# Performance work log

Hardware: AMD Instinct MI355X
Metric: run time of the kernel (lower is better)

## Reference

```python
import jax, jax.numpy as jnp
import numpy as np

B, N, D = 4, 2048, 1024

def setup_inputs() -> dict:
    key = jax.random.key(0)
    ks = jax.random.split(key, 8)
    s = 1.0 / np.sqrt(D)
    return {
        "x": jax.random.normal(ks[0], (B, N, D), dtype=jnp.float32),
        "Wq": jax.random.normal(ks[1], (D, D), dtype=jnp.float32) * s,
        "bq": jnp.zeros((D,), dtype=jnp.float32),
        "Wk": jax.random.normal(ks[2], (D, D), dtype=jnp.float32) * s,
        "bk": jnp.zeros((D,), dtype=jnp.float32),
        "Wv": jax.random.normal(ks[3], (D, D), dtype=jnp.float32) * s,
        "bv": jnp.zeros((D,), dtype=jnp.float32),
        "gamma": jnp.ones((1,), dtype=jnp.float32),
    }

def reference(x, Wq, bq, Wk, bk, Wv, bv, gamma):
    d = x.shape[-1]
    delta = 1.0 / jnp.sqrt(jnp.asarray(d, dtype=x.dtype))
    # torch Linear: y = x @ W.T + b, W is [out, in]
    Q = jnp.einsum('bnd,ed->bne', x, Wq) + bq
    K = jnp.einsum('bnd,ed->bne', x, Wk) + bk
    V = jnp.einsum('bnd,ed->bne', x, Wv) + bv
    scores = jnp.einsum('bne,bme->bnm', Q, K) * delta  # [B, N, N]
    attn = jax.nn.softmax(scores, axis=-1)
    out = jnp.einsum('bnm,bme->bne', attn, V)
    return out * gamma + x
```

## Files before the change

kernel.cpp:

```cpp
#include <hip/hip_runtime.h>

typedef _Float16 f16;
typedef __attribute__((ext_vector_type(4))) _Float16 f16x4;
typedef __attribute__((ext_vector_type(8))) _Float16 f16x8;
typedef __attribute__((ext_vector_type(4))) float f32x4;

#define B_ 4
#define N_ 2048
#define D_ 1024

__global__ __launch_bounds__(256) void k_cast_all(const float4* __restrict__ x,
                                                  const float4* __restrict__ wq,
                                                  const float4* __restrict__ wk,
                                                  const float4* __restrict__ wv,
                                                  f16x4* __restrict__ xo,
                                                  f16x4* __restrict__ wqo,
                                                  f16x4* __restrict__ wko,
                                                  f16x4* __restrict__ wvo,
                                                  float* __restrict__ rowsum) {
  int b = blockIdx.x;
  if (b >= 11264) {
    rowsum[(b - 11264) * 256 + threadIdx.x] = 0.f;
    return;
  }
  const float4* in;
  f16x4* out;
  int idx;
  if (b < 8192)       { in = x;  out = xo;  idx = b * 256 + threadIdx.x; }
  else if (b < 9216)  { in = wq; out = wqo; idx = (b - 8192) * 256 + threadIdx.x; }
  else if (b < 10240) { in = wk; out = wko; idx = (b - 9216) * 256 + threadIdx.x; }
  else                { in = wv; out = wvo; idx = (b - 10240) * 256 + threadIdx.x; }
  float4 v = in[idx];
  f16x4 o = { (_Float16)v.x, (_Float16)v.y, (_Float16)v.z, (_Float16)v.w };
  out[idx] = o;
}

__device__ __forceinline__ void stage_tile(const char* gRowBase, int rowStrideBytes,
                                           int kByte, char* lds, int tid) {
#pragma unroll
  for (int it = 0; it < 4; ++it) {
    int lin = it * 4096 + tid * 16;
    int row = lin >> 7;
    int pchunk = (lin >> 4) & 7;
    int lchunk = pchunk ^ (row & 7);
    const char* g = gRowBase + (long)row * rowStrideBytes + kByte + lchunk * 16;
    char* l = lds + it * 4096 + ((tid >> 6) << 10);
    __builtin_amdgcn_global_load_lds(
        (const __attribute__((address_space(1))) unsigned int*)g,
        (__attribute__((address_space(3))) unsigned int*)l, 16, 0, 0);
  }
}

__device__ __forceinline__ void gemm_mainloop(const f16* __restrict__ A, int lda,
                                              const f16* __restrict__ B, int ldb,
                                              int K, char* ldsA, char* ldsB,
                                              f32x4 acc[4][4]) {
  const int tid = threadIdx.x;
  const int lane = tid & 63, wave = tid >> 6;
  const int wm = wave >> 1, wn = wave & 1;
  const int quad = lane >> 4, l16 = lane & 15;
  const char* Ab = (const char*)A;
  const char* Bb = (const char*)B;
  const int nK = K >> 6;
  for (int ks = 0; ks < nK; ++ks) {
    __syncthreads();
    stage_tile(Ab, lda * 2, ks * 128, ldsA, tid);
    stage_tile(Bb, ldb * 2, ks * 128, ldsB, tid);
    __syncthreads();
#pragma unroll
    for (int kk = 0; kk < 2; ++kk) {
      f16x8 af[4], bfv[4];
#pragma unroll
      for (int i = 0; i < 4; ++i) {
        int c = kk * 4 + quad;
        int rA = wm * 64 + i * 16 + l16;
        af[i] = *(const f16x8*)(ldsA + rA * 128 + ((c ^ (rA & 7)) << 4));
        int rB = wn * 64 + i * 16 + l16;
        bfv[i] = *(const f16x8*)(ldsB + rB * 128 + ((c ^ (rB & 7)) << 4));
      }
#pragma unroll
      for (int i = 0; i < 4; ++i)
#pragma unroll
        for (int j = 0; j < 4; ++j)
          acc[i][j] = __builtin_amdgcn_mfma_f32_16x16x32_f16(af[i], bfv[j], acc[i][j], 0, 0, 0);
    }
  }
}

__global__ __launch_bounds__(256, 2) void k_qkv(const f16* __restrict__ X,
                                                const f16* __restrict__ Wq,
                                                const f16* __restrict__ Wk,
                                                const f16* __restrict__ Wv,
                                                const float* __restrict__ bq,
                                                const float* __restrict__ bk,
                                                const float* __restrict__ bv,
                                                f16* __restrict__ Q, f16* __restrict__ Ko,
                                                f16* __restrict__ Vt) {
  __shared__ __align__(16) char lds[65536];
  char* ldsX = lds;
  int fid = blockIdx.x + 8 * blockIdx.y;
  int c_ = fid & 7, k_ = fid >> 3;
  int lx = k_ & 7;
  int ly = c_ * 8 + (k_ >> 3);
  int tm = ly * 128, tn = lx * 128;
  const int tid = threadIdx.x;
  const int lane = tid & 63, wave = tid >> 6;
  const int wm = wave >> 1, wn = wave & 1;
  const int quad = lane >> 4, l16 = lane & 15;
  f32x4 acc[3][4][4];
#pragma unroll
  for (int w = 0; w < 3; ++w)
#pragma unroll
    for (int i = 0; i < 4; ++i)
#pragma unroll
      for (int j = 0; j < 4; ++j) acc[w][i][j] = (f32x4){0.f, 0.f, 0.f, 0.f};

  const char* Xb = (const char*)(X + (long)tm * D_);
  const char* Wb[3] = { (const char*)(Wq + (long)tn * D_),
                        (const char*)(Wk + (long)tn * D_),
                        (const char*)(Wv + (long)tn * D_) };
  for (int ks = 0; ks < (D_ >> 6); ++ks) {
    __syncthreads();
    stage_tile(Xb, D_ * 2, ks * 128, ldsX, tid);
#pragma unroll
    for (int w = 0; w < 3; ++w) stage_tile(Wb[w], D_ * 2, ks * 128, lds + 16384 * (w + 1), tid);
    __syncthreads();
#pragma unroll
    for (int kk = 0; kk < 2; ++kk) {
      f16x8 af[4];
#pragma unroll
      for (int i = 0; i < 4; ++i) {
        int c = kk * 4 + quad;
        int rA = wm * 64 + i * 16 + l16;
        af[i] = *(const f16x8*)(ldsX + rA * 128 + ((c ^ (rA & 7)) << 4));
      }
#pragma unroll
      for (int w = 0; w < 3; ++w) {
        f16x8 bfv[4];
#pragma unroll
        for (int j = 0; j < 4; ++j) {
          int c = kk * 4 + quad;
          int rB = wn * 64 + j * 16 + l16;
          bfv[j] = *(const f16x8*)(lds + 16384 * (w + 1) + rB * 128 + ((c ^ (rB & 7)) << 4));
        }
#pragma unroll
        for (int i = 0; i < 4; ++i)
#pragma unroll
          for (int j = 0; j < 4; ++j)
            acc[w][i][j] = __builtin_amdgcn_mfma_f32_16x16x32_f16(af[i], bfv[j], acc[w][i][j], 0, 0, 0);
      }
    }
  }

  const float* biases[2] = { bq, bk };
  f16* outs[2] = { Q, Ko };
#pragma unroll
  for (int w = 0; w < 2; ++w) {
    f16* out = outs[w];
#pragma unroll
    for (int j = 0; j < 4; ++j) {
      int col = tn + wn * 64 + j * 16 + l16;
      float bb = biases[w][col];
#pragma unroll
      for (int i = 0; i < 4; ++i) {
        int rbase = tm + wm * 64 + i * 16 + quad * 4;
#pragma unroll
        for (int r = 0; r < 4; ++r)
          out[(long)(rbase + r) * D_ + col] = (_Float16)(acc[w][i][j][r] + bb);
      }
    }
  }

  __syncthreads();
  f16* ldsT = (f16*)lds;
#pragma unroll
  for (int j = 0; j < 4; ++j) {
    int cl = wn * 64 + j * 16 + l16;
    float bb = bv[tn + cl];
#pragma unroll
    for (int i = 0; i < 4; ++i) {
      int rl = wm * 64 + i * 16 + quad * 4;
      f16x4 p = { (_Float16)(acc[2][i][j][0] + bb), (_Float16)(acc[2][i][j][1] + bb),
                  (_Float16)(acc[2][i][j][2] + bb), (_Float16)(acc[2][i][j][3] + bb) };
      *(f16x4*)(ldsT + cl * 136 + rl) = p;
    }
  }
  __syncthreads();
  int bb_ = tm >> 11, nbase = tm & 2047;
  f16* VtB = Vt + (long)bb_ * D_ * N_ + nbase;
#pragma unroll
  for (int it = 0; it < 8; ++it) {
    int f = it * 16 + (tid >> 4);
    int c = tid & 15;
    f16x8 v = *(const f16x8*)(ldsT + f * 136 + c * 8);
    *(f16x8*)(VtB + (long)(tn + f) * N_ + c * 8) = v;
  }
}

__global__ __launch_bounds__(256) void k_scores(const f16* __restrict__ Q,
                                                const f16* __restrict__ Kf,
                                                f16* __restrict__ S,
                                                float* __restrict__ rowsum) {
  __shared__ __align__(16) char lds[36864];
  int b = blockIdx.z;
  int fid = blockIdx.x + 16 * blockIdx.y;
  int c_ = fid & 7, k_ = fid >> 3;
  int lx = 4 * (c_ & 3) + (k_ & 3);
  int ly = 8 * (c_ >> 2) + (k_ >> 2);
  int tm = ly * 128, tn = lx * 128;
  const f16* A = Q + (long)b * N_ * D_ + (long)tm * D_;
  const f16* Bm = Kf + (long)b * N_ * D_ + (long)tn * D_;
  f32x4 acc[4][4];
#pragma unroll
  for (int i = 0; i < 4; ++i)
#pragma unroll
    for (int j = 0; j < 4; ++j) acc[i][j] = (f32x4){0.f, 0.f, 0.f, 0.f};
  gemm_mainloop(A, D_, Bm, D_, D_, lds, lds + 16384, acc);
  f16* Sb = S + (long)b * N_ * N_;
  const float delta = 0.03125f;
  int tid = threadIdx.x, lane = tid & 63, wave = tid >> 6;
  int wm = wave >> 1, wn = wave & 1, quad = lane >> 4, l16 = lane & 15;

  __syncthreads();
  f16* ldsS = (f16*)lds;
  float rsum[4][4];
#pragma unroll
  for (int i = 0; i < 4; ++i)
#pragma unroll
    for (int r = 0; r < 4; ++r) rsum[i][r] = 0.f;
#pragma unroll
  for (int j = 0; j < 4; ++j) {
    int col = wn * 64 + j * 16 + l16;
#pragma unroll
    for (int i = 0; i < 4; ++i) {
      int rbase = wm * 64 + i * 16 + quad * 4;
#pragma unroll
      for (int r = 0; r < 4; ++r) {
        float e = __expf(acc[i][j][r] * delta);
        rsum[i][r] += e;
        ldsS[(rbase + r) * 136 + col] = (_Float16)e;
      }
    }
  }
#pragma unroll
  for (int m = 1; m < 16; m <<= 1)
#pragma unroll
    for (int i = 0; i < 4; ++i)
#pragma unroll
      for (int r = 0; r < 4; ++r) rsum[i][r] += __shfl_xor(rsum[i][r], m);
  if (l16 == 0) {
    float* rs = rowsum + (long)b * N_ + tm;
#pragma unroll
    for (int i = 0; i < 4; ++i)
#pragma unroll
      for (int r = 0; r < 4; ++r)
        atomicAdd(rs + wm * 64 + i * 16 + quad * 4 + r, rsum[i][r]);
  }
  __syncthreads();
  int rloc = tid >> 4, c = tid & 15;
#pragma unroll
  for (int p = 0; p < 8; ++p) {
    int row = p * 16 + rloc;
    f16x8 v = *(const f16x8*)((const char*)ldsS + row * 272 + c * 16);
    *(f16x8*)(Sb + (long)(tm + row) * N_ + tn + c * 8) = v;
  }
}

__global__ __launch_bounds__(256) void k_out(const f16* __restrict__ P,
                                             const f16* __restrict__ Vt,
                                             const f16* __restrict__ xf,
                                             const float* __restrict__ gamma,
                                             const float* __restrict__ rowsum,
                                             float* __restrict__ out) {
  __shared__ __align__(16) char ldsA[16384];
  __shared__ __align__(16) char ldsB[16384];
  int b = blockIdx.z;
  int fid = blockIdx.x + 8 * blockIdx.y;
  int c_ = fid & 7, k_ = fid >> 3;
  int lx = 4 * (c_ & 1) + (k_ & 3);
  int ly = 4 * (c_ >> 1) + (k_ >> 2);
  int tm = ly * 128, tn = lx * 128;
  const f16* A = P + (long)b * N_ * N_ + (long)tm * N_;
  const f16* Bm = Vt + (long)b * D_ * N_ + (long)tn * N_;
  f32x4 acc[4][4];
#pragma unroll
  for (int i = 0; i < 4; ++i)
#pragma unroll
    for (int j = 0; j < 4; ++j) acc[i][j] = (f32x4){0.f, 0.f, 0.f, 0.f};
  gemm_mainloop(A, N_, Bm, N_, N_, ldsA, ldsB, acc);
  float g = gamma[0];
  int tid = threadIdx.x, lane = tid & 63, wave = tid >> 6;
  int wm = wave >> 1, wn = wave & 1, quad = lane >> 4, l16 = lane & 15;
  float inv[4][4];
#pragma unroll
  for (int i = 0; i < 4; ++i)
#pragma unroll
    for (int r = 0; r < 4; ++r)
      inv[i][r] = g / rowsum[(long)b * N_ + tm + wm * 64 + i * 16 + quad * 4 + r];
#pragma unroll
  for (int j = 0; j < 4; ++j) {
    int col = tn + wn * 64 + j * 16 + l16;
#pragma unroll
    for (int i = 0; i < 4; ++i) {
      int rbase = tm + wm * 64 + i * 16 + quad * 4;
#pragma unroll
      for (int r = 0; r < 4; ++r) {
        long idx = (long)b * N_ * D_ + (long)(rbase + r) * D_ + col;
        out[idx] = acc[i][j][r] * inv[i][r] + (float)xf[idx];
      }
    }
  }
}

extern "C" void kernel_launch(void* const* d_in, const int* in_sizes, int n_in,
                              void* d_out, int out_size, void* d_ws, size_t ws_size,
                              hipStream_t stream) {
  const float* x  = (const float*)d_in[0];
  const float* Wq = (const float*)d_in[1];
  const float* bq = (const float*)d_in[2];
  const float* Wk = (const float*)d_in[3];
  const float* bk = (const float*)d_in[4];
  const float* Wv = (const float*)d_in[5];
  const float* bv = (const float*)d_in[6];
  const float* gamma = (const float*)d_in[7];
  float* out = (float*)d_out;
  char* ws = (char*)d_ws;

  f16* Qb  = (f16*)(ws);
  f16* Kb  = (f16*)(ws + (16u << 20));
  f16* Vt  = (f16*)(ws + (32u << 20));
  f16* Xb  = (f16*)(ws + (48u << 20));
  f16* Wqb = (f16*)(ws + (64u << 20));
  f16* Wkb = (f16*)(ws + (66u << 20));
  f16* Wvb = (f16*)(ws + (68u << 20));
  f16* S   = (f16*)(ws + (64u << 20));
  float* rowsum = (float*)(ws + (96u << 20));

  k_cast_all<<<11296, 256, 0, stream>>>((const float4*)x, (const float4*)Wq,
                                        (const float4*)Wk, (const float4*)Wv,
                                        (f16x4*)Xb, (f16x4*)Wqb, (f16x4*)Wkb, (f16x4*)Wvb,
                                        rowsum);
  k_qkv<<<dim3(8, 64), 256, 0, stream>>>(Xb, Wqb, Wkb, Wvb, bq, bk, bv, Qb, Kb, Vt);
  k_scores<<<dim3(16, 16, 4), 256, 0, stream>>>(Qb, Kb, S, rowsum);
  k_out<<<dim3(8, 16, 4), 256, 0, stream>>>(S, Vt, Xb, gamma, rowsum, out);
}
```

Measured before the change: 263.0 us.

## Pipeline GEMM mainloops with triple-buffered async LDS loads and 256-wide tiles

Replaces the synchronous single-buffer GEMM loop with a three-stage pipeline. Async global-to-LDS loads for future K-steps are issued while MFMAs run, gated by vmcnt waits and raw barriers, and s_setprio is raised around the MFMA blocks. All three GEMM kernels move to 512-thread blocks. QKV and scores use 256x256 tiles, and the output GEMM uses 256x128 tiles with XCD-aware block remapping. QKV is split into separate Q/K/V blocks instead of one fused block, and the epilogues write through LDS in two passes. This aims to hide load latency and raise MFMA density, at the cost of more LDS, register pressure and fragile hand-written waitcnt logic.

```diff
diff --git a/kernel.cpp b/kernel.cpp
--- a/kernel.cpp
+++ b/kernel.cpp
@@ -35,59 +35,133 @@
   out[idx] = o;
 }
 
-__device__ __forceinline__ void stage_tile(const char* gRowBase, int rowStrideBytes,
-                                           int kByte, char* lds, int tid) {
-#pragma unroll
-  for (int it = 0; it < 4; ++it) {
-    int lin = it * 4096 + tid * 16;
-    int row = lin >> 7;
-    int pchunk = (lin >> 4) & 7;
-    int lchunk = pchunk ^ (row & 7);
-    const char* g = gRowBase + (long)row * rowStrideBytes + kByte + lchunk * 16;
-    char* l = lds + it * 4096 + ((tid >> 6) << 10);
-    __builtin_amdgcn_global_load_lds(
-        (const __attribute__((address_space(1))) unsigned int*)g,
-        (__attribute__((address_space(3))) unsigned int*)l, 16, 0, 0);
-  }
-}
-
-__device__ __forceinline__ void gemm_mainloop(const f16* __restrict__ A, int lda,
-                                              const f16* __restrict__ B, int ldb,
-                                              int K, char* ldsA, char* ldsB,
-                                              f32x4 acc[4][4]) {
+__device__ __forceinline__ void stage32(const char* g0, int ldBytes, int kByte,
+                                        char* slot, int tid, int nrounds) {
+#pragma unroll
+  for (int r = 0; r < 2; ++r) {
+    if (r < nrounds) {
+      int lin = r * 8192 + tid * 16;
+      int row = lin >> 6;
+      int lch = ((lin >> 4) & 3) ^ (row & 3);
+      const char* g = g0 + (long)row * ldBytes + kByte + lch * 16;
+      char* l = slot + r * 8192 + ((tid >> 6) << 10);
+      __builtin_amdgcn_global_load_lds(
+          (const __attribute__((address_space(1))) unsigned int*)g,
+          (__attribute__((address_space(3))) unsigned int*)l, 16, 0, 0);
+    }
+  }
+}
+
+__device__ __forceinline__ void gemm_pipe256(const char* gA, int ldaB,
+                                             const char* gB, int ldbB,
+                                             int nK, char* lds, f32x4 acc[8][4]) {
+  const int tid = threadIdx.x;
+  const int lane = tid & 63, wave = tid >> 6;
+  const int wm = wave >> 2, wn = wave & 3;
+  const int quad = lane >> 4, l16 = lane & 15;
+  stage32(gA, ldaB, 0, lds, tid, 2);
+  stage32(gB, ldbB, 0, lds + 16384, tid, 2);
+  stage32(gA, ldaB, 64, lds + 32768, tid, 2);
+  stage32(gB, ldbB, 64, lds + 49152, tid, 2);
+  int cs = 0;
+  for (int t = 0; t < nK; ++t) {
+    char* sA = lds + cs * 32768;
+    char* sB = sA + 16384;
+    int ns = cs - 1; if (ns < 0) ns = 2;
+    char* nA = lds + ns * 32768;
+    const bool st = (t + 2 < nK);
+    const int kB = (t + 2) << 6;
+    if (t + 1 < nK) asm volatile("s_waitcnt vmcnt(4)" ::: "memory");
+    else            asm volatile("s_waitcnt vmcnt(0)" ::: "memory");
+    __builtin_amdgcn_s_barrier();
+    f16x8 af[4], bf[4];
+#pragma unroll
+    for (int i = 0; i < 4; ++i) {
+      int rA = wm * 128 + i * 16 + l16;
+      af[i] = *(const f16x8*)(sA + rA * 64 + ((quad ^ (rA & 3)) << 4));
+    }
+#pragma unroll
+    for (int j = 0; j < 4; ++j) {
+      int rB = wn * 64 + j * 16 + l16;
+      bf[j] = *(const f16x8*)(sB + rB * 64 + ((quad ^ (rB & 3)) << 4));
+    }
+    if (st) stage32(gA, ldaB, kB, nA, tid, 2);
+    __builtin_amdgcn_s_barrier();
+    __builtin_amdgcn_s_setprio(1);
+#pragma unroll
+    for (int i = 0; i < 4; ++i)
+#pragma unroll
+      for (int j = 0; j < 4; ++j)
+        acc[i][j] = __builtin_amdgcn_mfma_f32_16x16x32_f16(af[i], bf[j], acc[i][j], 0, 0, 0);
+    __builtin_amdgcn_s_setprio(0);
+    __builtin_amdgcn_s_barrier();
+#pragma unroll
+    for (int i = 0; i < 4; ++i) {
+      int rA = wm * 128 + (i + 4) * 16 + l16;
+      af[i] = *(const f16x8*)(sA + rA * 64 + ((quad ^ (rA & 3)) << 4));
+    }
+    if (st) stage32(gB, ldbB, kB, nA + 16384, tid, 2);
+    __builtin_amdgcn_s_barrier();
+    __builtin_amdgcn_s_setprio(1);
+#pragma unroll
+    for (int i = 0; i < 4; ++i)
+#pragma unroll
+      for (int j = 0; j < 4; ++j)
+        acc[i + 4][j] = __builtin_amdgcn_mfma_f32_16x16x32_f16(af[i], bf[j], acc[i + 4][j], 0, 0, 0);
+    __builtin_amdgcn_s_setprio(0);
+    cs = (cs == 2) ? 0 : cs + 1;
+  }
+  __builtin_amdgcn_s_barrier();
+}
+
+__device__ __forceinline__ void gemm_pipe128(const char* gA, int ldaB,
+                                             const char* gB, int ldbB,
+                                             int nK, char* lds, f32x4 acc[4][4]) {
   const int tid = threadIdx.x;
   const int lane = tid & 63, wave = tid >> 6;
   const int wm = wave >> 1, wn = wave & 1;
   const int quad = lane >> 4, l16 = lane & 15;
-  const char* Ab = (const char*)A;
-  const char* Bb = (const char*)B;
-  const int nK = K >> 6;
-  for (int ks = 0; ks < nK; ++ks) {
-    __syncthreads();
-    stage_tile(Ab, lda * 2, ks * 128, ldsA, tid);
-    stage_tile(Bb, ldb * 2, ks * 128, ldsB, tid);
-    __syncthreads();
-#pragma unroll
-    for (int kk = 0; kk < 2; ++kk) {
-      f16x8 af[4], bfv[4];
-#pragma unroll
-      for (int i = 0; i < 4; ++i) {
-        int c = kk * 4 + quad;
-        int rA = wm * 64 + i * 16 + l16;
-        af[i] = *(const f16x8*)(ldsA + rA * 128 + ((c ^ (rA & 7)) << 4));
-        int rB = wn * 64 + i * 16 + l16;
-        bfv[i] = *(const f16x8*)(ldsB + rB * 128 + ((c ^ (rB & 7)) << 4));
-      }
-#pragma unroll
-      for (int i = 0; i < 4; ++i)
-#pragma unroll
-        for (int j = 0; j < 4; ++j)
-          acc[i][j] = __builtin_amdgcn_mfma_f32_16x16x32_f16(af[i], bfv[j], acc[i][j], 0, 0, 0);
-    }
-  }
-}
-
-__global__ __launch_bounds__(256, 2) void k_qkv(const f16* __restrict__ X,
+  stage32(gA, ldaB, 0, lds, tid, 2);
+  stage32(gB, ldbB, 0, lds + 16384, tid, 1);
+  stage32(gA, ldaB, 64, lds + 24576, tid, 2);
+  stage32(gB, ldbB, 64, lds + 40960, tid, 1);
+  int cs = 0;
+  for (int t = 0; t < nK; ++t) {
+    char* sA = lds + cs * 24576;
+    char* sB = sA + 16384;
+    int ns = cs - 1; if (ns < 0) ns = 2;
+    char* nA = lds + ns * 24576;
+    const bool st = (t + 2 < nK);
+    const int kB = (t + 2) << 6;
+    if (t + 1 < nK) asm volatile("s_waitcnt vmcnt(3)" ::: "memory");
+    else            asm volatile("s_waitcnt vmcnt(0)" ::: "memory");
+    __builtin_amdgcn_s_barrier();
+    f16x8 af[4], bf[4];
+#pragma unroll
+    for (int i = 0; i < 4; ++i) {
+      int rA = wm * 64 + i * 16 + l16;
+      af[i] = *(const f16x8*)(sA + rA * 64 + ((quad ^ (rA & 3)) << 4));
+    }
+#pragma unroll
+    for (int j = 0; j < 4; ++j) {
+      int rB = wn * 64 + j * 16 + l16;
+      bf[j] = *(const f16x8*)(sB + rB * 64 + ((quad ^ (rB & 3)) << 4));
+    }
+    if (st) { stage32(gA, ldaB, kB, nA, tid, 2); stage32(gB, ldbB, kB, nA + 16384, tid, 1); }
+    __builtin_amdgcn_s_barrier();
+    __builtin_amdgcn_s_setprio(1);
+#pragma unroll
+    for (int i = 0; i < 4; ++i)
+#pragma unroll
+      for (int j = 0; j < 4; ++j)
+        acc[i][j] = __builtin_amdgcn_mfma_f32_16x16x32_f16(af[i], bf[j], acc[i][j], 0, 0, 0);
+    __builtin_amdgcn_s_setprio(0);
+    cs = (cs == 2) ? 0 : cs + 1;
+  }
+  __builtin_amdgcn_s_barrier();
+}
+
+__global__ __launch_bounds__(512, 2) void k_qkv(const f16* __restrict__ X,
                                                 const f16* __restrict__ Wq,
                                                 const f16* __restrict__ Wk,
                                                 const f16* __restrict__ Wv,
@@ -96,201 +170,177 @@
                                                 const float* __restrict__ bv,
                                                 f16* __restrict__ Q, f16* __restrict__ Ko,
                                                 f16* __restrict__ Vt) {
-  __shared__ __align__(16) char lds[65536];
-  char* ldsX = lds;
-  int fid = blockIdx.x + 8 * blockIdx.y;
-  int c_ = fid & 7, k_ = fid >> 3;
-  int lx = k_ & 7;
-  int ly = c_ * 8 + (k_ >> 3);
-  int tm = ly * 128, tn = lx * 128;
-  const int tid = threadIdx.x;
-  const int lane = tid & 63, wave = tid >> 6;
-  const int wm = wave >> 1, wn = wave & 1;
-  const int quad = lane >> 4, l16 = lane & 15;
-  f32x4 acc[3][4][4];
-#pragma unroll
-  for (int w = 0; w < 3; ++w)
-#pragma unroll
-    for (int i = 0; i < 4; ++i)
-#pragma unroll
-      for (int j = 0; j < 4; ++j) acc[w][i][j] = (f32x4){0.f, 0.f, 0.f, 0.f};
-
-  const char* Xb = (const char*)(X + (long)tm * D_);
-  const char* Wb[3] = { (const char*)(Wq + (long)tn * D_),
-                        (const char*)(Wk + (long)tn * D_),
-                        (const char*)(Wv + (long)tn * D_) };
-  for (int ks = 0; ks < (D_ >> 6); ++ks) {
-    __syncthreads();
-    stage_tile(Xb, D_ * 2, ks * 128, ldsX, tid);
-#pragma unroll
-    for (int w = 0; w < 3; ++w) stage_tile(Wb[w], D_ * 2, ks * 128, lds + 16384 * (w + 1), tid);
-    __syncthreads();
-#pragma unroll
-    for (int kk = 0; kk < 2; ++kk) {
-      f16x8 af[4];
-#pragma unroll
-      for (int i = 0; i < 4; ++i) {
-        int c = kk * 4 + quad;
-        int rA = wm * 64 + i * 16 + l16;
-        af[i] = *(const f16x8*)(ldsX + rA * 128 + ((c ^ (rA & 7)) << 4));
-      }
-#pragma unroll
-      for (int w = 0; w < 3; ++w) {
-        f16x8 bfv[4];
-#pragma unroll
-        for (int j = 0; j < 4; ++j) {
-          int c = kk * 4 + quad;
-          int rB = wn * 64 + j * 16 + l16;
-          bfv[j] = *(const f16x8*)(lds + 16384 * (w + 1) + rB * 128 + ((c ^ (rB & 7)) << 4));
-        }
-#pragma unroll
-        for (int i = 0; i < 4; ++i)
-#pragma unroll
-          for (int j = 0; j < 4; ++j)
-            acc[w][i][j] = __builtin_amdgcn_mfma_f32_16x16x32_f16(af[i], bfv[j], acc[w][i][j], 0, 0, 0);
-      }
-    }
-  }
-
-  const float* biases[2] = { bq, bk };
-  f16* outs[2] = { Q, Ko };
-#pragma unroll
-  for (int w = 0; w < 2; ++w) {
-    f16* out = outs[w];
+  __shared__ __align__(16) char lds[98304];
+  int fid = blockIdx.x;
+  int xcd = fid & 7, k = fid >> 3;
+  int rowt = xcd * 4 + (k & 3);
+  int colt = k >> 2;
+  int tm = rowt * 256;
+  int w = colt >> 2;
+  int tn = (colt & 3) * 256;
+  const f16* Wsel = (w == 0) ? Wq : (w == 1) ? Wk : Wv;
+  f32x4 acc[8][4];
+#pragma unroll
+  for (int i = 0; i < 8; ++i)
+#pragma unroll
+    for (int j = 0; j < 4; ++j) acc[i][j] = (f32x4){0.f, 0.f, 0.f, 0.f};
+  gemm_pipe256((const char*)(X + (long)tm * D_), D_ * 2,
+               (const char*)(Wsel + (long)tn * D_), D_ * 2, D_ / 32, lds, acc);
+  const int tid = threadIdx.x;
+  const int lane = tid & 63, wave = tid >> 6;
+  const int wm = wave >> 2, wn = wave & 3;
+  const int quad = lane >> 4, l16 = lane & 15;
+  if (w < 2) {
+    const float* bias = w ? bk : bq;
+    f16* out = w ? Ko : Q;
 #pragma unroll
     for (int j = 0; j < 4; ++j) {
       int col = tn + wn * 64 + j * 16 + l16;
-      float bb = biases[w][col];
-#pragma unroll
-      for (int i = 0; i < 4; ++i) {
-        int rbase = tm + wm * 64 + i * 16 + quad * 4;
+      float bb = bias[col];
+#pragma unroll
+      for (int i = 0; i < 8; ++i) {
+        int rbase = tm + wm * 128 + i * 16 + quad * 4;
 #pragma unroll
         for (int r = 0; r < 4; ++r)
-          out[(long)(rbase + r) * D_ + col] = (_Float16)(acc[w][i][j][r] + bb);
-      }
-    }
-  }
-
-  __syncthreads();
-  f16* ldsT = (f16*)lds;
-#pragma unroll
-  for (int j = 0; j < 4; ++j) {
-    int cl = wn * 64 + j * 16 + l16;
-    float bb = bv[tn + cl];
-#pragma unroll
-    for (int i = 0; i < 4; ++i) {
-      int rl = wm * 64 + i * 16 + quad * 4;
-      f16x4 p = { (_Float16)(acc[2][i][j][0] + bb), (_Float16)(acc[2][i][j][1] + bb),
-                  (_Float16)(acc[2][i][j][2] + bb), (_Float16)(acc[2][i][j][3] + bb) };
-      *(f16x4*)(ldsT + cl * 136 + rl) = p;
-    }
-  }
-  __syncthreads();
-  int bb_ = tm >> 11, nbase = tm & 2047;
-  f16* VtB = Vt + (long)bb_ * D_ * N_ + nbase;
-#pragma unroll
-  for (int it = 0; it < 8; ++it) {
-    int f = it * 16 + (tid >> 4);
-    int c = tid & 15;
-    f16x8 v = *(const f16x8*)(ldsT + f * 136 + c * 8);
-    *(f16x8*)(VtB + (long)(tn + f) * N_ + c * 8) = v;
-  }
-}
-
-__global__ __launch_bounds__(256) void k_scores(const f16* __restrict__ Q,
-                                                const f16* __restrict__ Kf,
-                                                f16* __restrict__ S,
-                                                float* __restrict__ rowsum) {
-  __shared__ __align__(16) char lds[36864];
-  int b = blockIdx.z;
-  int fid = blockIdx.x + 16 * blockIdx.y;
-  int c_ = fid & 7, k_ = fid >> 3;
-  int lx = 4 * (c_ & 3) + (k_ & 3);
-  int ly = 8 * (c_ >> 2) + (k_ >> 2);
-  int tm = ly * 128, tn = lx * 128;
-  const f16* A = Q + (long)b * N_ * D_ + (long)tm * D_;
-  const f16* Bm = Kf + (long)b * N_ * D_ + (long)tn * D_;
-  f32x4 acc[4][4];
-#pragma unroll
-  for (int i = 0; i < 4; ++i)
+          out[(long)(rbase + r) * D_ + col] = (_Float16)(acc[i][j][r] + bb);
+      }
+    }
+  } else {
+    int bidx = tm >> 11, ntok = tm & 2047;
+    f16* VtB = Vt + (long)bidx * D_ * N_ + ntok;
+    f16* ldsT = (f16*)lds;
+    for (int pass = 0; pass < 2; ++pass) {
+      __builtin_amdgcn_s_barrier();
+      if ((wn >> 1) == pass) {
+        int wnl = wn & 1;
+#pragma unroll
+        for (int j = 0; j < 4; ++j) {
+          int cl = wnl * 64 + j * 16 + l16;
+          float bb = bv[tn + pass * 128 + cl];
+#pragma unroll
+          for (int i = 0; i < 8; ++i) {
+            int rl = wm * 128 + i * 16 + quad * 4;
+            f16x4 p = { (_Float16)(acc[i][j][0] + bb), (_Float16)(acc[i][j][1] + bb),
+                        (_Float16)(acc[i][j][2] + bb), (_Float16)(acc[i][j][3] + bb) };
+            *(f16x4*)(ldsT + cl * 264 + rl) = p;
+          }
+        }
+      }
+      __builtin_amdgcn_s_barrier();
+#pragma unroll
+      for (int p = 0; p < 8; ++p) {
+        int f = p * 16 + (tid >> 5);
+        int c = tid & 31;
+        f16x8 v = *(const f16x8*)(ldsT + f * 264 + c * 8);
+        *(f16x8*)(VtB + (long)(tn + pass * 128 + f) * N_ + c * 8) = v;
+      }
+    }
+  }
+}
+
+__global__ __launch_bounds__(512, 2) void k_scores(const f16* __restrict__ Qf,
+                                                   const f16* __restrict__ Kf,
+                                                   f16* __restrict__ S,
+                                                   float* __restrict__ rowsum) {
+  __shared__ __align__(16) char lds[98304];
+  int fid = blockIdx.x;
+  int xcd = fid & 7, k = fid >> 3;
+  int lin = xcd * 32 + k;
+  int b = lin >> 6;
+  int t = lin & 63;
+  int rowt = t & 7, colt = t >> 3;
+  int tm = rowt * 256, tn = colt * 256;
+  f32x4 acc[8][4];
+#pragma unroll
+  for (int i = 0; i < 8; ++i)
 #pragma unroll
     for (int j = 0; j < 4; ++j) acc[i][j] = (f32x4){0.f, 0.f, 0.f, 0.f};
-  gemm_mainloop(A, D_, Bm, D_, D_, lds, lds + 16384, acc);
+  gemm_pipe256((const char*)(Qf + (long)b * N_ * D_ + (long)tm * D_), D_ * 2,
+               (const char*)(Kf + (long)b * N_ * D_ + (long)tn * D_), D_ * 2,
+               D_ / 32, lds, acc);
+  const int tid = threadIdx.x;
+  const int lane = tid & 63, wave = tid >> 6;
+  const int wm = wave >> 2, wn = wave & 3;
+  const int quad = lane >> 4, l16 = lane & 15;
   f16* Sb = S + (long)b * N_ * N_;
   const float delta = 0.03125f;
-  int tid = threadIdx.x, lane = tid & 63, wave = tid >> 6;
-  int wm = wave >> 1, wn = wave & 1, quad = lane >> 4, l16 = lane & 15;
-
-  __syncthreads();
   f16* ldsS = (f16*)lds;
-  float rsum[4][4];
-#pragma unroll
-  for (int i = 0; i < 4; ++i)
+  float rsum[8][4];
+#pragma unroll
+  for (int i = 0; i < 8; ++i)
 #pragma unroll
     for (int r = 0; r < 4; ++r) rsum[i][r] = 0.f;
-#pragma unroll
-  for (int j = 0; j < 4; ++j) {
-    int col = wn * 64 + j * 16 + l16;
-#pragma unroll
-    for (int i = 0; i < 4; ++i) {
-      int rbase = wm * 64 + i * 16 + quad * 4;
-#pragma unroll
-      for (int r = 0; r < 4; ++r) {
-        float e = __expf(acc[i][j][r] * delta);
-        rsum[i][r] += e;
-        ldsS[(rbase + r) * 136 + col] = (_Float16)e;
-      }
+  for (int pass = 0; pass < 2; ++pass) {
+    __builtin_amdgcn_s_barrier();
+    if ((wn >> 1) == pass) {
+      int wnl = wn & 1;
+#pragma unroll
+      for (int j = 0; j < 4; ++j) {
+        int col = wnl * 64 + j * 16 + l16;
+#pragma unroll
+        for (int i = 0; i < 8; ++i) {
+          int rbase = wm * 128 + i * 16 + quad * 4;
+#pragma unroll
+          for (int r = 0; r < 4; ++r) {
+            float e = __expf(acc[i][j][r] * delta);
+            rsum[i][r] += e;
+            ldsS[(rbase + r) * 136 + col] = (_Float16)e;
+          }
+        }
+      }
+    }
+    __builtin_amdgcn_s_barrier();
+#pragma unroll
+    for (int p = 0; p < 8; ++p) {
+      int row = p * 32 + (tid >> 4);
+      int c = tid & 15;
+      f16x8 v = *(const f16x8*)(ldsS + row * 136 + c * 8);
+      *(f16x8*)(Sb + (long)(tm + row) * N_ + tn + pass * 128 + c * 8) = v;
     }
   }
 #pragma unroll
   for (int m = 1; m < 16; m <<= 1)
 #pragma unroll
-    for (int i = 0; i < 4; ++i)
+    for (int i = 0; i < 8; ++i)
 #pragma unroll
       for (int r = 0; r < 4; ++r) rsum[i][r] += __shfl_xor(rsum[i][r], m);
   if (l16 == 0) {
     float* rs = rowsum + (long)b * N_ + tm;
 #pragma unroll
-    for (int i = 0; i < 4; ++i)
+    for (int i = 0; i < 8; ++i)
 #pragma unroll
       for (int r = 0; r < 4; ++r)
-        atomicAdd(rs + wm * 64 + i * 16 + quad * 4 + r, rsum[i][r]);
-  }
-  __syncthreads();
-  int rloc = tid >> 4, c = tid & 15;
-#pragma unroll
-  for (int p = 0; p < 8; ++p) {
-    int row = p * 16 + rloc;
-    f16x8 v = *(const f16x8*)((const char*)ldsS + row * 272 + c * 16);
-    *(f16x8*)(Sb + (long)(tm + row) * N_ + tn + c * 8) = v;
-  }
-}
-
-__global__ __launch_bounds__(256) void k_out(const f16* __restrict__ P,
-                                             const f16* __restrict__ Vt,
-                                             const f16* __restrict__ xf,
-                                             const float* __restrict__ gamma,
-                                             const float* __restrict__ rowsum,
-                                             float* __restrict__ out) {
-  __shared__ __align__(16) char ldsA[16384];
-  __shared__ __align__(16) char ldsB[16384];
-  int b = blockIdx.z;
-  int fid = blockIdx.x + 8 * blockIdx.y;
-  int c_ = fid & 7, k_ = fid >> 3;
-  int lx = 4 * (c_ & 1) + (k_ & 3);
-  int ly = 4 * (c_ >> 1) + (k_ >> 2);
-  int tm = ly * 128, tn = lx * 128;
-  const f16* A = P + (long)b * N_ * N_ + (long)tm * N_;
-  const f16* Bm = Vt + (long)b * D_ * N_ + (long)tn * N_;
+        atomicAdd(rs + wm * 128 + i * 16 + quad * 4 + r, rsum[i][r]);
+  }
+}
+
+__global__ __launch_bounds__(512, 2) void k_out(const f16* __restrict__ P,
+                                                const f16* __restrict__ Vt,
+                                                const f16* __restrict__ xf,
+                                                const float* __restrict__ gamma,
+                                                const float* __restrict__ rowsum,
+                                                float* __restrict__ out) {
+  __shared__ __align__(16) char lds[73728];
+  int fid = blockIdx.x;
+  int xcd = fid & 7, kq = fid >> 3;
+  int lin = xcd * 32 + kq;
+  int b = lin >> 6;
+  int t = lin & 63;
+  int rowt = t >> 3, colt = t & 7;
+  int tm = rowt * 256, tn = colt * 128;
   f32x4 acc[4][4];
 #pragma unroll
   for (int i = 0; i < 4; ++i)
 #pragma unroll
     for (int j = 0; j < 4; ++j) acc[i][j] = (f32x4){0.f, 0.f, 0.f, 0.f};
-  gemm_mainloop(A, N_, Bm, N_, N_, ldsA, ldsB, acc);
+  gemm_pipe128((const char*)(P + (long)b * N_ * N_ + (long)tm * N_), N_ * 2,
+               (const char*)(Vt + (long)b * D_ * N_ + (long)tn * N_), N_ * 2,
+               N_ / 32, lds, acc);
+  const int tid = threadIdx.x;
+  const int lane = tid & 63, wave = tid >> 6;
+  const int wm = wave >> 1, wn = wave & 1;
+  const int quad = lane >> 4, l16 = lane & 15;
   float g = gamma[0];
-  int tid = threadIdx.x, lane = tid & 63, wave = tid >> 6;
-  int wm = wave >> 1, wn = wave & 1, quad = lane >> 4, l16 = lane & 15;
   float inv[4][4];
 #pragma unroll
   for (int i = 0; i < 4; ++i)
@@ -340,7 +390,7 @@
                                         (const float4*)Wk, (const float4*)Wv,
                                         (f16x4*)Xb, (f16x4*)Wqb, (f16x4*)Wkb, (f16x4*)Wvb,
                                         rowsum);
-  k_qkv<<<dim3(8, 64), 256, 0, stream>>>(Xb, Wqb, Wkb, Wvb, bq, bk, bv, Qb, Kb, Vt);
-  k_scores<<<dim3(16, 16, 4), 256, 0, stream>>>(Qb, Kb, S, rowsum);
-  k_out<<<dim3(8, 16, 4), 256, 0, stream>>>(S, Vt, Xb, gamma, rowsum, out);
-}
+  k_qkv<<<384, 512, 0, stream>>>(Xb, Wqb, Wkb, Wvb, bq, bk, bv, Qb, Kb, Vt);
+  k_scores<<<256, 512, 0, stream>>>(Qb, Kb, S, rowsum);
+  k_out<<<256, 512, 0, stream>>>(S, Vt, Xb, gamma, rowsum, out);
+}
```

Result: slower. 300.5 us (+14.3%).
